# Kernel tuning notes

Hardware: AMD Instinct MI355X
Metric: run time of the kernel (lower is better)

Reference implementation:

```python
import jax, jax.numpy as jnp
import numpy as np

B, T, D = 2, 2048, 1024
H, G, K = 16, 4, 64          # num_heads, num_kv_heads, head_dim
R = H // G                   # GQA repeat factor
F = 4096                     # mlp_dim
EPS = 1e-6


def rms_norm(x, scale, eps=EPS):
    var = jnp.mean(x.astype(jnp.float32) ** 2, axis=-1, keepdims=True)
    normed = x * jax.lax.rsqrt(var + eps)
    return (scale * normed).astype(x.dtype)


def apply_rope(x_BTHK, sin_BTK, cos_BTK):
    half = x_BTHK.shape[-1] // 2
    x1, x2 = x_BTHK[..., :half], x_BTHK[..., half:]
    s = sin_BTK[:, :, None, :]
    c = cos_BTK[:, :, None, :]
    return jnp.concatenate([x1 * c - x2 * s, x2 * c + x1 * s], axis=-1).astype(x_BTHK.dtype)


def setup_inputs() -> dict:
    key = jax.random.key(0)
    ks = jax.random.split(key, 12)
    hidden_BTD = jax.random.normal(ks[0], (B, T, D), jnp.float32)
    # rope tables: realistic sin/cos of position*inv_freq
    inv_freq = 1.0 / (10000.0 ** (jnp.arange(K // 2, dtype=jnp.float32) / (K // 2)))
    ang = jnp.arange(T, dtype=jnp.float32)[:, None] * inv_freq[None, :]  # [T, K/2]
    sin_BTK = jnp.broadcast_to(jnp.sin(ang)[None], (B, T, K // 2))
    cos_BTK = jnp.broadcast_to(jnp.cos(ang)[None], (B, T, K // 2))
    mask = jnp.broadcast_to(jnp.tril(jnp.ones((T, T), bool))[None], (B, T, T))
    sc = 1.0 / np.sqrt(D)
    scf = 1.0 / np.sqrt(F)
    return {
        "hidden_BTD": hidden_BTD, "sin_BTK": sin_BTK, "cos_BTK": cos_BTK, "mask": mask,
        "ln1_scale": jnp.ones((D,), jnp.float32),
        "ln2_scale": jnp.ones((D,), jnp.float32),
        "qn_scale": jnp.ones((K,), jnp.float32),
        "kn_scale": jnp.ones((K,), jnp.float32),
        "q_w": jax.random.normal(ks[1], (D, H * K), jnp.float32) * sc,
        "k_w": jax.random.normal(ks[2], (D, G * K), jnp.float32) * sc,
        "v_w": jax.random.normal(ks[3], (D, G * K), jnp.float32) * sc,
        "o_w": jax.random.normal(ks[4], (H * K, D), jnp.float32) * sc,
        "gate_w": jax.random.normal(ks[5], (D, F), jnp.float32) * sc,
        "up_w": jax.random.normal(ks[6], (D, F), jnp.float32) * sc,
        "down_w": jax.random.normal(ks[7], (F, D), jnp.float32) * scf,
    }


def reference(hidden_BTD, sin_BTK, cos_BTK, mask, ln1_scale, ln2_scale,
              qn_scale, kn_scale, q_w, k_w, v_w, o_w, gate_w, up_w, down_w):
    x = rms_norm(hidden_BTD, ln1_scale)
    q = rms_norm((x @ q_w).reshape(B, T, H, K), qn_scale)
    k = rms_norm((x @ k_w).reshape(B, T, G, K), kn_scale)
    v = (x @ v_w).reshape(B, T, G, K)
    q = apply_rope(q, sin_BTK, cos_BTK)
    k = apply_rope(k, sin_BTK, cos_BTK)
    q_BTGRK = q.reshape(B, T, G, R, K)
    scale = K ** (-0.5)
    logits = jnp.einsum('BTGRK,BSGK->BTSGR', q_BTGRK, k) * scale
    neg = float(jnp.finfo(logits.dtype).min)
    logits = jnp.where(mask[:, :, :, None, None], logits, neg)
    weights = jax.nn.softmax(logits.astype(jnp.float32), axis=2).astype(logits.dtype)
    attn = jnp.einsum('BTSGR,BSGK->BTGRK', weights, v).reshape(B, T, H * K)
    hidden_BTD = hidden_BTD + attn @ o_w
    y = rms_norm(hidden_BTD, ln2_scale)
    ff = (jax.nn.silu(y @ gate_w) * (y @ up_w)) @ down_w
    return hidden_BTD + ff
```

## Files before the change

kernel.cpp:

```cpp
#include <hip/hip_runtime.h>
#include <hip/hip_bf16.h>

#define EPSF 1e-6f
constexpr int Bsz  = 2;
constexpr int Tseq = 2048;
constexpr int Dmod = 1024;
constexpr int Hh   = 16;
constexpr int Gg   = 4;
constexpr int Ff   = 4096;
constexpr int Mrows = Bsz * Tseq;

typedef __attribute__((ext_vector_type(8))) short bf16x8;
typedef __attribute__((ext_vector_type(4))) float f32x4;
typedef unsigned short u16;

__device__ inline u16 f2bf(float x) {
    union { float f; unsigned u; } v; v.f = x;
    unsigned r = v.u + 0x7fff + ((v.u >> 16) & 1);
    return (u16)(r >> 16);
}
__device__ inline float bf2f(u16 h) {
    union { unsigned u; float f; } v; v.u = ((unsigned)h) << 16; return v.f;
}

__device__ __forceinline__ void async_copy16(const u16* g, u16* l) {
    __builtin_amdgcn_global_load_lds(
        (const __attribute__((address_space(1))) void*)g,
        (__attribute__((address_space(3))) void*)l, 16, 0, 0);
}


__global__ __launch_bounds__(256) void wprep_all_kernel(
    const float* __restrict__ q_w, const float* __restrict__ k_w,
    const float* __restrict__ v_w, const float* __restrict__ o_w,
    const float* __restrict__ gate_w, const float* __restrict__ up_w,
    const float* __restrict__ down_w,
    u16* __restrict__ QKVT, u16* __restrict__ OTh, u16* __restrict__ OTl,
    u16* __restrict__ GTh, u16* __restrict__ UTh, u16* __restrict__ DTh)
{
    const int bx = blockIdx.x;
    const float* W; u16* Th; u16* Tl = nullptr;
    int N, Kd, ntile, ktile, drow;
    if (bx < 1024) {
        W = q_w; N = 1024; Kd = 1024; ntile = bx & 31; ktile = bx >> 5;
        Th = QKVT; drow = ntile * 32;
    } else if (bx < 1280) {
        const int i = bx - 1024;
        W = k_w; N = 256; Kd = 1024; ntile = i & 7; ktile = i >> 3;
        Th = QKVT; drow = 1024 + ntile * 32;
    } else if (bx < 1536) {
        const int i = bx - 1280;
        W = v_w; N = 256; Kd = 1024; ntile = i & 7; ktile = i >> 3;
        Th = QKVT; drow = 1280 + ntile * 32;
    } else if (bx < 2560) {
        const int i = bx - 1536;
        W = o_w; N = 1024; Kd = 1024; ntile = i & 31; ktile = i >> 5;
        Th = OTh; Tl = OTl; drow = ntile * 32;
    } else if (bx < 6656) {
        const int i = bx - 2560;
        W = gate_w; N = 4096; Kd = 1024; ntile = i & 127; ktile = i >> 7;
        Th = GTh; drow = ntile * 32;
    } else if (bx < 10752) {
        const int i = bx - 6656;
        W = up_w; N = 4096; Kd = 1024; ntile = i & 127; ktile = i >> 7;
        Th = UTh; drow = ntile * 32;
    } else {
        const int i = bx - 10752;
        W = down_w; N = 1024; Kd = 4096; ntile = i & 31; ktile = i >> 5;
        Th = DTh; drow = ntile * 32;
    }
    const int n0 = ntile * 32, k0 = ktile * 32;

    __shared__ float tile[32][33];
    const int r = threadIdx.x >> 3, c4 = (threadIdx.x & 7) * 4;
    const float4 v = *reinterpret_cast<const float4*>(&W[(size_t)(k0 + r) * N + n0 + c4]);
    tile[r][c4 + 0] = v.x; tile[r][c4 + 1] = v.y;
    tile[r][c4 + 2] = v.z; tile[r][c4 + 3] = v.w;
    __syncthreads();
    const int nl = threadIdx.x >> 3, kq = (threadIdx.x & 7) * 4;
    float x0 = tile[kq + 0][nl], x1 = tile[kq + 1][nl];
    float x2 = tile[kq + 2][nl], x3 = tile[kq + 3][nl];
    ushort4 h;
    h.x = f2bf(x0); h.y = f2bf(x1); h.z = f2bf(x2); h.w = f2bf(x3);
    *reinterpret_cast<ushort4*>(&Th[(size_t)(drow + nl) * Kd + k0 + kq]) = h;
    if (Tl) {
        ushort4 l;
        l.x = f2bf(x0 - bf2f(h.x)); l.y = f2bf(x1 - bf2f(h.y));
        l.z = f2bf(x2 - bf2f(h.z)); l.w = f2bf(x3 - bf2f(h.w));
        *reinterpret_cast<ushort4*>(&Tl[(size_t)(drow + nl) * Kd + k0 + kq]) = l;
    }
}

template <int LO>
__global__ __launch_bounds__(256) void rmsnorm_split_kernel(
    const float* __restrict__ x, const float* __restrict__ scale,
    u16* __restrict__ oh, u16* __restrict__ ol)
{
    const int row = blockIdx.x;
    const int tid = threadIdx.x;
    const float4 v = reinterpret_cast<const float4*>(x + (size_t)row * Dmod)[tid];
    float ss = v.x * v.x + v.y * v.y + v.z * v.z + v.w * v.w;
    #pragma unroll
    for (int off = 32; off; off >>= 1) ss += __shfl_xor(ss, off, 64);
    __shared__ float part[4];
    if ((tid & 63) == 0) part[tid >> 6] = ss;
    __syncthreads();
    const float tot = part[0] + part[1] + part[2] + part[3];
    const float rstd = rsqrtf(tot * (1.0f / Dmod) + EPSF);
    const float4 sc = reinterpret_cast<const float4*>(scale)[tid];
    float o0 = v.x * rstd * sc.x, o1 = v.y * rstd * sc.y;
    float o2 = v.z * rstd * sc.z, o3 = v.w * rstd * sc.w;
    ushort4 h;
    h.x = f2bf(o0); h.y = f2bf(o1); h.z = f2bf(o2); h.w = f2bf(o3);
    *reinterpret_cast<ushort4*>(&oh[(size_t)row * Dmod + tid * 4]) = h;
    if (LO) {
        ushort4 l;
        l.x = f2bf(o0 - bf2f(h.x)); l.y = f2bf(o1 - bf2f(h.y));
        l.z = f2bf(o2 - bf2f(h.z)); l.w = f2bf(o3 - bf2f(h.w));
        *reinterpret_cast<ushort4*>(&ol[(size_t)row * Dmod + tid * 4]) = l;
    }
}

template <int ASPLIT, int BSPLIT, int RES>
__global__ __launch_bounds__(256, 2) void mfma_gemm_kernel(
    const u16* __restrict__ Ah, const u16* __restrict__ Al,
    const u16* __restrict__ Bh, const u16* __restrict__ Bl,
    const float* __restrict__ res, float* __restrict__ C,
    int M, int N, int Kd)
{
    __shared__ u16 As_h[128 * 32];
    __shared__ u16 As_l[128 * 32];
    __shared__ u16 Bs_h[128 * 32];
    __shared__ u16 Bs_l[128 * 32];

    const int tid = threadIdx.x;
    const int lane = tid & 63, wave = tid >> 6;
    const int wm = (wave >> 1) * 64, wn = (wave & 1) * 64;
    const int m0 = blockIdx.y * 128, n0 = blockIdx.x * 128;
    const int fm = lane & 15, quad = lane >> 4;
    const int fsw = (fm >> 1) & 3;
    const int fcol = ((quad ^ fsw) * 8);

    f32x4 acc[4][4];
    #pragma unroll
    for (int i = 0; i < 4; ++i)
        #pragma unroll
        for (int j = 0; j < 4; ++j) acc[i][j] = (f32x4){0.f, 0.f, 0.f, 0.f};

    const int lrow = lane >> 2;
    const int lchunk = lane & 3;
    const int schunk = lchunk ^ ((lrow >> 1) & 3);

    for (int k0 = 0; k0 < Kd; k0 += 32) {
        __syncthreads();
        #pragma unroll
        for (int p = 0; p < 2; ++p) {
            const int row = wave * 32 + p * 16 + lrow;
            const size_t ga = (size_t)(m0 + row) * Kd + k0 + schunk * 8;
            const size_t gb = (size_t)(n0 + row) * Kd + k0 + schunk * 8;
            const int ls = row * 32 + lchunk * 8;
            async_copy16(&Ah[ga], &As_h[ls]);
            if (ASPLIT) async_copy16(&Al[ga], &As_l[ls]);
            async_copy16(&Bh[gb], &Bs_h[ls]);
            if (BSPLIT) async_copy16(&Bl[gb], &Bs_l[ls]);
        }
        __syncthreads();

        bf16x8 ah[4], al[4], bh[4], bl[4];
        #pragma unroll
        for (int t = 0; t < 4; ++t) {
            const int ra = (wm + t * 16 + fm) * 32 + fcol;
            const int rb = (wn + t * 16 + fm) * 32 + fcol;
            ah[t] = *reinterpret_cast<const bf16x8*>(&As_h[ra]);
            bh[t] = *reinterpret_cast<const bf16x8*>(&Bs_h[rb]);
            if (ASPLIT) al[t] = *reinterpret_cast<const bf16x8*>(&As_l[ra]);
            if (BSPLIT) bl[t] = *reinterpret_cast<const bf16x8*>(&Bs_l[rb]);
        }
        #pragma unroll
        for (int mt = 0; mt < 4; ++mt)
            #pragma unroll
            for (int nt = 0; nt < 4; ++nt) {
                acc[mt][nt] = __builtin_amdgcn_mfma_f32_16x16x32_bf16(
                    ah[mt], bh[nt], acc[mt][nt], 0, 0, 0);
                if (BSPLIT)
                    acc[mt][nt] = __builtin_amdgcn_mfma_f32_16x16x32_bf16(
                        ah[mt], bl[nt], acc[mt][nt], 0, 0, 0);
                if (ASPLIT)
                    acc[mt][nt] = __builtin_amdgcn_mfma_f32_16x16x32_bf16(
                        al[mt], bh[nt], acc[mt][nt], 0, 0, 0);
            }
    }

    const int cr = (lane >> 4) * 4, cn = lane & 15;
    #pragma unroll
    for (int mt = 0; mt < 4; ++mt)
        #pragma unroll
        for (int nt = 0; nt < 4; ++nt)
            #pragma unroll
            for (int r = 0; r < 4; ++r) {
                const int gm = m0 + wm + mt * 16 + cr + r;
                const int gn = n0 + wn + nt * 16 + cn;
                float v = acc[mt][nt][r];
                if (RES) v += res[(size_t)gm * N + gn];
                C[(size_t)gm * N + gn] = v;
            }
}

__global__ __launch_bounds__(256, 2) void qkv_fused_kernel(
    const u16* __restrict__ Ah, const u16* __restrict__ Bh,
    const float* __restrict__ qn, const float* __restrict__ kn,
    const float* __restrict__ sinp, const float* __restrict__ cosp,
    u16* __restrict__ Qbh, u16* __restrict__ Qbl,
    u16* __restrict__ Kbh, u16* __restrict__ Kbl,
    u16* __restrict__ Vth, u16* __restrict__ Vtl)
{
    __shared__ u16 As_h[128 * 32];
    __shared__ u16 Bs_h[128 * 32];

    const int Kd = 1024;
    const int tid = threadIdx.x;
    const int lane = tid & 63, wave = tid >> 6;
    const int wm = (wave >> 1) * 64, wn = (wave & 1) * 64;
    const int m0 = blockIdx.y * 128, n0 = blockIdx.x * 128;
    const int fm = lane & 15, quad = lane >> 4;
    const int fsw = (fm >> 1) & 3;
    const int fcol = ((quad ^ fsw) * 8);

    f32x4 acc[4][4];
    #pragma unroll
    for (int i = 0; i < 4; ++i)
        #pragma unroll
        for (int j = 0; j < 4; ++j) acc[i][j] = (f32x4){0.f, 0.f, 0.f, 0.f};

    const int lrow = lane >> 2;
    const int lchunk = lane & 3;
    const int schunk = lchunk ^ ((lrow >> 1) & 3);

    for (int k0 = 0; k0 < Kd; k0 += 32) {
        __syncthreads();
        #pragma unroll
        for (int p = 0; p < 2; ++p) {
            const int row = wave * 32 + p * 16 + lrow;
            const size_t ga = (size_t)(m0 + row) * Kd + k0 + schunk * 8;
            const size_t gb = (size_t)(n0 + row) * Kd + k0 + schunk * 8;
            const int ls = row * 32 + lchunk * 8;
            async_copy16(&Ah[ga], &As_h[ls]);
            async_copy16(&Bh[gb], &Bs_h[ls]);
        }
        __syncthreads();

        bf16x8 ah[4], bh[4];
        #pragma unroll
        for (int t = 0; t < 4; ++t) {
            ah[t] = *reinterpret_cast<const bf16x8*>(&As_h[(wm + t * 16 + fm) * 32 + fcol]);
            bh[t] = *reinterpret_cast<const bf16x8*>(&Bs_h[(wn + t * 16 + fm) * 32 + fcol]);
        }
        #pragma unroll
        for (int mt = 0; mt < 4; ++mt)
            #pragma unroll
            for (int nt = 0; nt < 4; ++nt)
                acc[mt][nt] = __builtin_amdgcn_mfma_f32_16x16x32_bf16(
                    ah[mt], bh[nt], acc[mt][nt], 0, 0, 0);
    }

    const int gn0 = n0 + wn;
    const int l15 = lane & 15;

    if (gn0 < 1280) {
        const bool isQ = (gn0 < 1024);
        const float* nsc = isQ ? qn : kn;
        const float osc = isQ ? 0.125f : 1.0f;
        u16* __restrict__ oh = isQ ? Qbh : Kbh;
        u16* __restrict__ ol = isQ ? Qbl : Kbl;
        const int rowstride = isQ ? 1024 : 256;
        const int colbase = isQ ? gn0 : gn0 - 1024;
        float sc[4];
        #pragma unroll
        for (int nt = 0; nt < 4; ++nt) sc[nt] = nsc[nt * 16 + l15];

        #pragma unroll
        for (int mt = 0; mt < 4; ++mt)
            #pragma unroll
            for (int r = 0; r < 4; ++r) {
                const int bt = m0 + wm + mt * 16 + quad * 4 + r;
                float v[4];
                #pragma unroll
                for (int nt = 0; nt < 4; ++nt) v[nt] = acc[mt][nt][r];
                float ss = v[0] * v[0] + v[1] * v[1] + v[2] * v[2] + v[3] * v[3];
                #pragma unroll
                for (int off = 1; off < 16; off <<= 1)
                    ss += __shfl_xor(ss, off, 16);
                const float rstd = rsqrtf(ss * (1.0f / 64.0f) + EPSF);
                float nv[4];
                #pragma unroll
                for (int nt = 0; nt < 4; ++nt) nv[nt] = v[nt] * rstd * sc[nt];
                const float s0 = sinp[bt * 32 + l15];
                const float c0 = cosp[bt * 32 + l15];
                const float s1 = sinp[bt * 32 + 16 + l15];
                const float c1 = cosp[bt * 32 + 16 + l15];
                float o[4];
                o[0] = (nv[0] * c0 - nv[2] * s0) * osc;
                o[1] = (nv[1] * c1 - nv[3] * s1) * osc;
                o[2] = (nv[2] * c0 + nv[0] * s0) * osc;
                o[3] = (nv[3] * c1 + nv[1] * s1) * osc;
                #pragma unroll
                for (int nt = 0; nt < 4; ++nt) {
                    const size_t off = (size_t)bt * rowstride + colbase + nt * 16 + l15;
                    const u16 hi = f2bf(o[nt]);
                    oh[off] = hi;
                    ol[off] = f2bf(o[nt] - bf2f(hi));
                }
            }
    } else {
        const int g = (gn0 - 1280) >> 6;
        const int b = (m0 + wm) >> 11;
        const int tb = ((m0 + wm) & 2047) + quad * 4;
        #pragma unroll
        for (int mt = 0; mt < 4; ++mt)
            #pragma unroll
            for (int nt = 0; nt < 4; ++nt) {
                const float v0 = acc[mt][nt][0], v1 = acc[mt][nt][1];
                const float v2 = acc[mt][nt][2], v3 = acc[mt][nt][3];
                ushort4 hv, lv;
                hv.x = f2bf(v0); hv.y = f2bf(v1); hv.z = f2bf(v2); hv.w = f2bf(v3);
                lv.x = f2bf(v0 - bf2f(hv.x)); lv.y = f2bf(v1 - bf2f(hv.y));
                lv.z = f2bf(v2 - bf2f(hv.z)); lv.w = f2bf(v3 - bf2f(hv.w));
                const size_t off =
                    ((size_t)((b * 4 + g) * 64 + nt * 16 + l15)) * Tseq + tb + mt * 16;
                *reinterpret_cast<ushort4*>(&Vth[off]) = hv;
                *reinterpret_cast<ushort4*>(&Vtl[off]) = lv;
            }
    }
}

__global__ __launch_bounds__(256, 2) void mfma_gateup_kernel(
    const u16* __restrict__ Ah, const u16* __restrict__ Al,
    const u16* __restrict__ Bg, const u16* __restrict__ Bu,
    u16* __restrict__ FF, int M, int N, int Kd)
{
    __shared__ u16 As_h[128 * 32];
    __shared__ u16 As_l[128 * 32];
    __shared__ u16 Gs[64 * 32];
    __shared__ u16 Us[64 * 32];

    const int tid = threadIdx.x;
    const int lane = tid & 63, wave = tid >> 6;
    const int wm = (wave >> 1) * 64, wn = (wave & 1) * 32;
    const int m0 = blockIdx.y * 128, n0 = blockIdx.x * 64;
    const int fm = lane & 15, quad = lane >> 4;
    const int fsw = (fm >> 1) & 3;
    const int fcol = ((quad ^ fsw) * 8);

    f32x4 accg[4][2], accu[4][2];
    #pragma unroll
    for (int i = 0; i < 4; ++i)
        #pragma unroll
        for (int j = 0; j < 2; ++j) {
            accg[i][j] = (f32x4){0.f, 0.f, 0.f, 0.f};
            accu[i][j] = (f32x4){0.f, 0.f, 0.f, 0.f};
        }

    const int lrow = lane >> 2;
    const int lchunk = lane & 3;
    const int schunk = lchunk ^ ((lrow >> 1) & 3);

    for (int k0 = 0; k0 < Kd; k0 += 32) {
        __syncthreads();
        #pragma unroll
        for (int p = 0; p < 2; ++p) {
            const int row = p * 64 + wave * 16 + lrow;
            const size_t ga = (size_t)(m0 + row) * Kd + k0 + schunk * 8;
            const int ls = row * 32 + lchunk * 8;
            async_copy16(&Ah[ga], &As_h[ls]);
            async_copy16(&Al[ga], &As_l[ls]);
        }
        {
            const int row = wave * 16 + lrow;
            const size_t gb = (size_t)(n0 + row) * Kd + k0 + schunk * 8;
            const int ls = row * 32 + lchunk * 8;
            async_copy16(&Bg[gb], &Gs[ls]);
            async_copy16(&Bu[gb], &Us[ls]);
        }
        __syncthreads();

        bf16x8 a_h[4], a_l[4], g_f[2], u_f[2];
        #pragma unroll
        for (int t = 0; t < 4; ++t) {
            const int ra = (wm + t * 16 + fm) * 32 + fcol;
            a_h[t] = *reinterpret_cast<const bf16x8*>(&As_h[ra]);
            a_l[t] = *reinterpret_cast<const bf16x8*>(&As_l[ra]);
        }
        #pragma unroll
        for (int j = 0; j < 2; ++j) {
            const int rb = (wn + j * 16 + fm) * 32 + fcol;
            g_f[j] = *reinterpret_cast<const bf16x8*>(&Gs[rb]);
            u_f[j] = *reinterpret_cast<const bf16x8*>(&Us[rb]);
        }
        #pragma unroll
        for (int mt = 0; mt < 4; ++mt)
            #pragma unroll
            for (int nt = 0; nt < 2; ++nt) {
                accg[mt][nt] = __builtin_amdgcn_mfma_f32_16x16x32_bf16(
                    a_h[mt], g_f[nt], accg[mt][nt], 0, 0, 0);
                accg[mt][nt] = __builtin_amdgcn_mfma_f32_16x16x32_bf16(
                    a_l[mt], g_f[nt], accg[mt][nt], 0, 0, 0);
                accu[mt][nt] = __builtin_amdgcn_mfma_f32_16x16x32_bf16(
                    a_h[mt], u_f[nt], accu[mt][nt], 0, 0, 0);
                accu[mt][nt] = __builtin_amdgcn_mfma_f32_16x16x32_bf16(
                    a_l[mt], u_f[nt], accu[mt][nt], 0, 0, 0);
            }
    }

    const int cr = (lane >> 4) * 4, cn = lane & 15;
    #pragma unroll
    for (int mt = 0; mt < 4; ++mt)
        #pragma unroll
        for (int nt = 0; nt < 2; ++nt)
            #pragma unroll
            for (int r = 0; r < 4; ++r) {
                const int gm = m0 + wm + mt * 16 + cr + r;
                const int gn = n0 + wn + nt * 16 + cn;
                const float g = accg[mt][nt][r];
                const float ff = (g / (1.0f + __expf(-g))) * accu[mt][nt][r];
                FF[(size_t)gm * N + gn] = f2bf(ff);
            }
}

__global__ __launch_bounds__(256) void attn_mfma_kernel(
    const u16* __restrict__ Qh, const u16* __restrict__ Ql,
    const u16* __restrict__ Kh, const u16* __restrict__ Kl,
    const u16* __restrict__ Vth, const u16* __restrict__ Vtl,
    u16* __restrict__ AOh, u16* __restrict__ AOl)
{
    __shared__ u16 KsH[64 * 72];
    __shared__ u16 KsL[64 * 72];
    __shared__ u16 VsH[64 * 72];
    __shared__ u16 VsL[64 * 72];
    __shared__ u16 Ps[4][16 * 72];

    const int tid = threadIdx.x;
    const int wave = tid >> 6, lane = tid & 63;
    const int l15 = lane & 15, quad = lane >> 4;

    const int bg = blockIdx.x & 7;
    const int b = bg >> 2, g = bg & 3;
    const int win = 127 - (blockIdx.x >> 3);
    const int t0 = win * 16;
    const int h = g * 4 + wave;

    bf16x8 qh[2], ql[2];
    {
        const size_t qrow = (size_t)(b * Tseq + t0 + l15) * 1024 + h * 64;
        #pragma unroll
        for (int ks = 0; ks < 2; ++ks) {
            qh[ks] = *reinterpret_cast<const bf16x8*>(&Qh[qrow + ks * 32 + quad * 8]);
            ql[ks] = *reinterpret_cast<const bf16x8*>(&Ql[qrow + ks * 32 + quad * 8]);
        }
    }

    const int srow = tid >> 2;
    const int scol = (tid & 3) * 16;
    const size_t kgb = (size_t)(b * Tseq) * 256 + g * 64 + scol;
    const size_t vgb = (size_t)(bg * 64 + srow) * Tseq + scol;

    const int nit = t0 / 64 + 1;

    uint4 ck0, ck1, cl0, cl1, cv0, cv1, cw0, cw1;
    {
        const size_t ka = kgb + (size_t)srow * 256;
        ck0 = *reinterpret_cast<const uint4*>(&Kh[ka]);
        ck1 = *reinterpret_cast<const uint4*>(&Kh[ka + 8]);
        cl0 = *reinterpret_cast<const uint4*>(&Kl[ka]);
        cl1 = *reinterpret_cast<const uint4*>(&Kl[ka + 8]);
        cv0 = *reinterpret_cast<const uint4*>(&Vth[vgb]);
        cv1 = *reinterpret_cast<const uint4*>(&Vth[vgb + 8]);
        cw0 = *reinterpret_cast<const uint4*>(&Vtl[vgb]);
        cw1 = *reinterpret_cast<const uint4*>(&Vtl[vgb + 8]);
    }

    f32x4 oacc[4];
    #pragma unroll
    for (int nt = 0; nt < 4; ++nt) oacc[nt] = (f32x4){0.f, 0.f, 0.f, 0.f};
    float m_r[4], l_r[4];
    #pragma unroll
    for (int r = 0; r < 4; ++r) { m_r[r] = -1e30f; l_r[r] = 0.0f; }

    u16* psw = &Ps[wave][0];
    const int lb = srow * 72 + scol;

    for (int it = 0; it < nit; ++it) {
        const int s0 = it * 64;
        const bool diag = (it == nit - 1);

        __syncthreads();
        *reinterpret_cast<uint4*>(&KsH[lb])     = ck0;
        *reinterpret_cast<uint4*>(&KsH[lb + 8]) = ck1;
        *reinterpret_cast<uint4*>(&KsL[lb])     = cl0;
        *reinterpret_cast<uint4*>(&KsL[lb + 8]) = cl1;
        *reinterpret_cast<uint4*>(&VsH[lb])     = cv0;
        *reinterpret_cast<uint4*>(&VsH[lb + 8]) = cv1;
        *reinterpret_cast<uint4*>(&VsL[lb])     = cw0;
        *reinterpret_cast<uint4*>(&VsL[lb + 8]) = cw1;
        if (it + 1 < nit) {
            const size_t ka = kgb + (size_t)(s0 + 64 + srow) * 256;
            ck0 = *reinterpret_cast<const uint4*>(&Kh[ka]);
            ck1 = *reinterpret_cast<const uint4*>(&Kh[ka + 8]);
            cl0 = *reinterpret_cast<const uint4*>(&Kl[ka]);
            cl1 = *reinterpret_cast<const uint4*>(&Kl[ka + 8]);
            const size_t va = vgb + s0 + 64;
            cv0 = *reinterpret_cast<const uint4*>(&Vth[va]);
            cv1 = *reinterpret_cast<const uint4*>(&Vth[va + 8]);
            cw0 = *reinterpret_cast<const uint4*>(&Vtl[va]);
            cw1 = *reinterpret_cast<const uint4*>(&Vtl[va + 8]);
        }
        __syncthreads();

        f32x4 sacc[4];
        #pragma unroll
        for (int nt = 0; nt < 4; ++nt) sacc[nt] = (f32x4){0.f, 0.f, 0.f, 0.f};

        #pragma unroll
        for (int ks = 0; ks < 2; ++ks) {
            bf16x8 kfh[4], kfl[4];
            #pragma unroll
            for (int nt = 0; nt < 4; ++nt) {
                const int a = (nt * 16 + l15) * 72 + ks * 32 + quad * 8;
                kfh[nt] = *reinterpret_cast<const bf16x8*>(&KsH[a]);
                kfl[nt] = *reinterpret_cast<const bf16x8*>(&KsL[a]);
            }
            #pragma unroll
            for (int nt = 0; nt < 4; ++nt) {
                sacc[nt] = __builtin_amdgcn_mfma_f32_16x16x32_bf16(qh[ks], kfh[nt], sacc[nt], 0, 0, 0);
                sacc[nt] = __builtin_amdgcn_mfma_f32_16x16x32_bf16(ql[ks], kfh[nt], sacc[nt], 0, 0, 0);
                sacc[nt] = __builtin_amdgcn_mfma_f32_16x16x32_bf16(qh[ks], kfl[nt], sacc[nt], 0, 0, 0);
            }
        }

        if (diag) {
            #pragma unroll
            for (int nt = 0; nt < 4; ++nt) {
                const int sg = s0 + nt * 16 + l15;
                #pragma unroll
                for (int r = 0; r < 4; ++r)
                    if (sg > t0 + quad * 4 + r) sacc[nt][r] = -1e30f;
            }
        }

        #pragma unroll
        for (int r = 0; r < 4; ++r) {
            float mx = fmaxf(fmaxf(sacc[0][r], sacc[1][r]),
                             fmaxf(sacc[2][r], sacc[3][r]));
            #pragma unroll
            for (int off = 1; off < 16; off <<= 1)
                mx = fmaxf(mx, __shfl_xor(mx, off, 16));
            const float mnew = fmaxf(m_r[r], mx);
            const float alpha = __expf(m_r[r] - mnew);
            m_r[r] = mnew;

            float rs = 0.0f;
            #pragma unroll
            for (int nt = 0; nt < 4; ++nt) {
                const float p = __expf(sacc[nt][r] - mnew);
                sacc[nt][r] = p;
                rs += p;
            }
            #pragma unroll
            for (int off = 1; off < 16; off <<= 1)
                rs += __shfl_xor(rs, off, 16);
            l_r[r] = l_r[r] * alpha + rs;
            #pragma unroll
            for (int nt = 0; nt < 4; ++nt) oacc[nt][r] *= alpha;
            #pragma unroll
            for (int nt = 0; nt < 4; ++nt)
                psw[(quad * 4 + r) * 72 + nt * 16 + l15] = f2bf(sacc[nt][r]);
        }

        #pragma unroll
        for (int ks = 0; ks < 2; ++ks) {
            const bf16x8 pa = *reinterpret_cast<const bf16x8*>(
                &psw[l15 * 72 + ks * 32 + quad * 8]);
            bf16x8 vfh[4], vfl[4];
            #pragma unroll
            for (int nt = 0; nt < 4; ++nt) {
                const int a = (nt * 16 + l15) * 72 + ks * 32 + quad * 8;
                vfh[nt] = *reinterpret_cast<const bf16x8*>(&VsH[a]);
                vfl[nt] = *reinterpret_cast<const bf16x8*>(&VsL[a]);
            }
            #pragma unroll
            for (int nt = 0; nt < 4; ++nt) {
                oacc[nt] = __builtin_amdgcn_mfma_f32_16x16x32_bf16(pa, vfh[nt], oacc[nt], 0, 0, 0);
                oacc[nt] = __builtin_amdgcn_mfma_f32_16x16x32_bf16(pa, vfl[nt], oacc[nt], 0, 0, 0);
            }
        }
    }

    #pragma unroll
    for (int r = 0; r < 4; ++r) {
        const float inv = 1.0f / l_r[r];
        const size_t orow = (size_t)(b * Tseq + t0 + quad * 4 + r) * 1024 + h * 64;
        #pragma unroll
        for (int nt = 0; nt < 4; ++nt) {
            const float o = oacc[nt][r] * inv;
            const u16 hi = f2bf(o);
            AOh[orow + nt * 16 + l15] = hi;
            AOl[orow + nt * 16 + l15] = f2bf(o - bf2f(hi));
        }
    }
}

extern "C" void kernel_launch(void* const* d_in, const int* in_sizes, int n_in,
                              void* d_out, int out_size, void* d_ws,
                              size_t ws_size, hipStream_t stream)
{
    const float* hidden = (const float*)d_in[0];
    const float* sinp   = (const float*)d_in[1];
    const float* cosp   = (const float*)d_in[2];
    const float* ln1    = (const float*)d_in[4];
    const float* ln2    = (const float*)d_in[5];
    const float* qn     = (const float*)d_in[6];
    const float* kn     = (const float*)d_in[7];
    const float* q_w    = (const float*)d_in[8];
    const float* k_w    = (const float*)d_in[9];
    const float* v_w    = (const float*)d_in[10];
    const float* o_w    = (const float*)d_in[11];
    const float* gate_w = (const float*)d_in[12];
    const float* up_w   = (const float*)d_in[13];
    const float* down_w = (const float*)d_in[14];
    float* out = (float*)d_out;

    char* base = (char*)d_ws;
    u16*   OTh  = (u16*)(base);
    u16*   OTl  = (u16*)(base + 2097152);
    u16*   GTh  = (u16*)(base + 4194304);
    u16*   UTh  = (u16*)(base + 12582912);
    u16*   DTh  = (u16*)(base + 20971520);
    u16*   QKVT = (u16*)(base + 29360128);
    u16*   Xh   = (u16*)(base + 32505856);
    u16*   Qbh  = (u16*)(base + 40894464);
    u16*   Qbl  = (u16*)(base + 49283072);
    u16*   Kbh  = (u16*)(base + 57671680);
    u16*   Kbl  = (u16*)(base + 59768832);
    u16*   Vth  = (u16*)(base + 61865984);
    u16*   Vtl  = (u16*)(base + 63963136);
    u16*   AOh  = (u16*)(base + 66060288);
    u16*   AOl  = (u16*)(base + 74448896);
    u16*   FFh  = (u16*)(base + 82837504);

    float* H2 = (float*)Qbh;
    u16*   Yh = Kbh;
    u16*   Yl = AOh;

    wprep_all_kernel<<<14848, 256, 0, stream>>>(
        q_w, k_w, v_w, o_w, gate_w, up_w, down_w,
        QKVT, OTh, OTl, GTh, UTh, DTh);

    rmsnorm_split_kernel<0><<<Mrows, 256, 0, stream>>>(hidden, ln1, Xh, nullptr);

    qkv_fused_kernel<<<dim3(12, 32), 256, 0, stream>>>(
        Xh, QKVT, qn, kn, sinp, cosp, Qbh, Qbl, Kbh, Kbl, Vth, Vtl);

    attn_mfma_kernel<<<Bsz * Gg * (Tseq / 16), 256, 0, stream>>>(
        Qbh, Qbl, Kbh, Kbl, Vth, Vtl, AOh, AOl);

    mfma_gemm_kernel<1, 1, 1><<<dim3(8, 32), 256, 0, stream>>>(
        AOh, AOl, OTh, OTl, hidden, H2, Mrows, Dmod, 1024);

    rmsnorm_split_kernel<1><<<Mrows, 256, 0, stream>>>(H2, ln2, Yh, Yl);

    mfma_gateup_kernel<<<dim3(Ff / 64, Mrows / 128), 256, 0, stream>>>(
        Yh, Yl, GTh, UTh, FFh, Mrows, Ff, 1024);

    mfma_gemm_kernel<0, 0, 1><<<dim3(8, 32), 256, 0, stream>>>(
        FFh, nullptr, DTh, nullptr, H2, out, Mrows, Dmod, 4096);
}
```

Before: 532.4 us.

## Narrow GEMM tiles to 128x64 and XOR-swizzle attention LDS with higher occupancy

The o-proj and down-proj GEMMs now use 128x64 output tiles, giving twice as many blocks (512 rather than 256) for better CU fill on the 1024-wide outputs. Their shared arrays for the unused low halves shrink when that split is off. The attention kernel drops its padded 72-stride LDS layout for a 64-stride XOR-swizzled layout for K, V and P, and raises launch bounds to 4 blocks per CU. The aim is lower LDS use and higher occupancy without bank conflicts. The trade-off is less data reuse per GEMM tile and possible register pressure from the tighter launch bound.

Result: slower. 625.2 us (+17.4%).

```diff
diff --git a/kernel.cpp b/kernel.cpp
--- a/kernel.cpp
+++ b/kernel.cpp
@@ -122,30 +122,30 @@
 }
 
 template <int ASPLIT, int BSPLIT, int RES>
-__global__ __launch_bounds__(256, 2) void mfma_gemm_kernel(
+__global__ __launch_bounds__(256, 2) void mfma_gemm64_kernel(
     const u16* __restrict__ Ah, const u16* __restrict__ Al,
     const u16* __restrict__ Bh, const u16* __restrict__ Bl,
     const float* __restrict__ res, float* __restrict__ C,
     int M, int N, int Kd)
 {
     __shared__ u16 As_h[128 * 32];
-    __shared__ u16 As_l[128 * 32];
-    __shared__ u16 Bs_h[128 * 32];
-    __shared__ u16 Bs_l[128 * 32];
+    __shared__ u16 As_l[ASPLIT ? 128 * 32 : 8];
+    __shared__ u16 Bs_h[64 * 32];
+    __shared__ u16 Bs_l[BSPLIT ? 64 * 32 : 8];
 
     const int tid = threadIdx.x;
     const int lane = tid & 63, wave = tid >> 6;
-    const int wm = (wave >> 1) * 64, wn = (wave & 1) * 64;
-    const int m0 = blockIdx.y * 128, n0 = blockIdx.x * 128;
+    const int wm = (wave >> 1) * 64, wn = (wave & 1) * 32;
+    const int m0 = blockIdx.y * 128, n0 = blockIdx.x * 64;
     const int fm = lane & 15, quad = lane >> 4;
     const int fsw = (fm >> 1) & 3;
     const int fcol = ((quad ^ fsw) * 8);
 
-    f32x4 acc[4][4];
+    f32x4 acc[4][2];
     #pragma unroll
     for (int i = 0; i < 4; ++i)
         #pragma unroll
-        for (int j = 0; j < 4; ++j) acc[i][j] = (f32x4){0.f, 0.f, 0.f, 0.f};
+        for (int j = 0; j < 2; ++j) acc[i][j] = (f32x4){0.f, 0.f, 0.f, 0.f};
 
     const int lrow = lane >> 2;
     const int lchunk = lane & 3;
@@ -155,39 +155,46 @@
         __syncthreads();
         #pragma unroll
         for (int p = 0; p < 2; ++p) {
-            const int row = wave * 32 + p * 16 + lrow;
+            const int row = p * 64 + wave * 16 + lrow;
             const size_t ga = (size_t)(m0 + row) * Kd + k0 + schunk * 8;
-            const size_t gb = (size_t)(n0 + row) * Kd + k0 + schunk * 8;
             const int ls = row * 32 + lchunk * 8;
             async_copy16(&Ah[ga], &As_h[ls]);
             if (ASPLIT) async_copy16(&Al[ga], &As_l[ls]);
+        }
+        {
+            const int row = wave * 16 + lrow;
+            const size_t gb = (size_t)(n0 + row) * Kd + k0 + schunk * 8;
+            const int ls = row * 32 + lchunk * 8;
             async_copy16(&Bh[gb], &Bs_h[ls]);
             if (BSPLIT) async_copy16(&Bl[gb], &Bs_l[ls]);
         }
         __syncthreads();
 
-        bf16x8 ah[4], al[4], bh[4], bl[4];
+        bf16x8 a_h[4], a_l[4], b_h[2], b_l[2];
         #pragma unroll
         for (int t = 0; t < 4; ++t) {
             const int ra = (wm + t * 16 + fm) * 32 + fcol;
-            const int rb = (wn + t * 16 + fm) * 32 + fcol;
-            ah[t] = *reinterpret_cast<const bf16x8*>(&As_h[ra]);
-            bh[t] = *reinterpret_cast<const bf16x8*>(&Bs_h[rb]);
-            if (ASPLIT) al[t] = *reinterpret_cast<const bf16x8*>(&As_l[ra]);
-            if (BSPLIT) bl[t] = *reinterpret_cast<const bf16x8*>(&Bs_l[rb]);
+            a_h[t] = *reinterpret_cast<const bf16x8*>(&As_h[ra]);
+            if (ASPLIT) a_l[t] = *reinterpret_cast<const bf16x8*>(&As_l[ra]);
+        }
+        #pragma unroll
+        for (int j = 0; j < 2; ++j) {
+            const int rb = (wn + j * 16 + fm) * 32 + fcol;
+            b_h[j] = *reinterpret_cast<const bf16x8*>(&Bs_h[rb]);
+            if (BSPLIT) b_l[j] = *reinterpret_cast<const bf16x8*>(&Bs_l[rb]);
         }
         #pragma unroll
         for (int mt = 0; mt < 4; ++mt)
             #pragma unroll
-            for (int nt = 0; nt < 4; ++nt) {
+            for (int nt = 0; nt < 2; ++nt) {
                 acc[mt][nt] = __builtin_amdgcn_mfma_f32_16x16x32_bf16(
-                    ah[mt], bh[nt], acc[mt][nt], 0, 0, 0);
+                    a_h[mt], b_h[nt], acc[mt][nt], 0, 0, 0);
                 if (BSPLIT)
                     acc[mt][nt] = __builtin_amdgcn_mfma_f32_16x16x32_bf16(
-                        ah[mt], bl[nt], acc[mt][nt], 0, 0, 0);
+                        a_h[mt], b_l[nt], acc[mt][nt], 0, 0, 0);
                 if (ASPLIT)
                     acc[mt][nt] = __builtin_amdgcn_mfma_f32_16x16x32_bf16(
-                        al[mt], bh[nt], acc[mt][nt], 0, 0, 0);
+                        a_l[mt], b_h[nt], acc[mt][nt], 0, 0, 0);
             }
     }
 
@@ -195,7 +202,7 @@
     #pragma unroll
     for (int mt = 0; mt < 4; ++mt)
         #pragma unroll
-        for (int nt = 0; nt < 4; ++nt)
+        for (int nt = 0; nt < 2; ++nt)
             #pragma unroll
             for (int r = 0; r < 4; ++r) {
                 const int gm = m0 + wm + mt * 16 + cr + r;
@@ -426,21 +433,22 @@
             }
 }
 
-__global__ __launch_bounds__(256) void attn_mfma_kernel(
+__global__ __launch_bounds__(256, 4) void attn_mfma_kernel(
     const u16* __restrict__ Qh, const u16* __restrict__ Ql,
     const u16* __restrict__ Kh, const u16* __restrict__ Kl,
     const u16* __restrict__ Vth, const u16* __restrict__ Vtl,
     u16* __restrict__ AOh, u16* __restrict__ AOl)
 {
-    __shared__ u16 KsH[64 * 72];
-    __shared__ u16 KsL[64 * 72];
-    __shared__ u16 VsH[64 * 72];
-    __shared__ u16 VsL[64 * 72];
-    __shared__ u16 Ps[4][16 * 72];
+    __shared__ u16 KsH[64 * 64];
+    __shared__ u16 KsL[64 * 64];
+    __shared__ u16 VsH[64 * 64];
+    __shared__ u16 VsL[64 * 64];
+    __shared__ u16 Ps[4][16 * 64];
 
     const int tid = threadIdx.x;
     const int wave = tid >> 6, lane = tid & 63;
     const int l15 = lane & 15, quad = lane >> 4;
+    const int fsw7 = l15 & 7;
 
     const int bg = blockIdx.x & 7;
     const int b = bg >> 2, g = bg & 3;
@@ -459,9 +467,12 @@
     }
 
     const int srow = tid >> 2;
-    const int scol = (tid & 3) * 16;
-    const size_t kgb = (size_t)(b * Tseq) * 256 + g * 64 + scol;
-    const size_t vgb = (size_t)(bg * 64 + srow) * Tseq + scol;
+    const int j2 = (tid & 3) * 2;
+    const int sw = srow & 7;
+    const int d0 = srow * 64 + ((j2    ) ^ sw) * 8;
+    const int d1 = srow * 64 + ((j2 + 1) ^ sw) * 8;
+    const size_t kgb = (size_t)(b * Tseq) * 256 + g * 64 + j2 * 8;
+    const size_t vgb = (size_t)(bg * 64 + srow) * Tseq + j2 * 8;
 
     const int nit = t0 / 64 + 1;
 
@@ -486,21 +497,20 @@
     for (int r = 0; r < 4; ++r) { m_r[r] = -1e30f; l_r[r] = 0.0f; }
 
     u16* psw = &Ps[wave][0];
-    const int lb = srow * 72 + scol;
 
     for (int it = 0; it < nit; ++it) {
         const int s0 = it * 64;
         const bool diag = (it == nit - 1);
 
         __syncthreads();
-        *reinterpret_cast<uint4*>(&KsH[lb])     = ck0;
-        *reinterpret_cast<uint4*>(&KsH[lb + 8]) = ck1;
-        *reinterpret_cast<uint4*>(&KsL[lb])     = cl0;
-        *reinterpret_cast<uint4*>(&KsL[lb + 8]) = cl1;
-        *reinterpret_cast<uint4*>(&VsH[lb])     = cv0;
-        *reinterpret_cast<uint4*>(&VsH[lb + 8]) = cv1;
-        *reinterpret_cast<uint4*>(&VsL[lb])     = cw0;
-        *reinterpret_cast<uint4*>(&VsL[lb + 8]) = cw1;
+        *reinterpret_cast<uint4*>(&KsH[d0]) = ck0;
+        *reinterpret_cast<uint4*>(&KsH[d1]) = ck1;
+        *reinterpret_cast<uint4*>(&KsL[d0]) = cl0;
+        *reinterpret_cast<uint4*>(&KsL[d1]) = cl1;
+        *reinterpret_cast<uint4*>(&VsH[d0]) = cv0;
+        *reinterpret_cast<uint4*>(&VsH[d1]) = cv1;
+        *reinterpret_cast<uint4*>(&VsL[d0]) = cw0;
+        *reinterpret_cast<uint4*>(&VsL[d1]) = cw1;
         if (it + 1 < nit) {
             const size_t ka = kgb + (size_t)(s0 + 64 + srow) * 256;
             ck0 = *reinterpret_cast<const uint4*>(&Kh[ka]);
@@ -521,10 +531,11 @@
 
         #pragma unroll
         for (int ks = 0; ks < 2; ++ks) {
+            const int pc = ((ks * 4 + quad) ^ fsw7) * 8;
             bf16x8 kfh[4], kfl[4];
             #pragma unroll
             for (int nt = 0; nt < 4; ++nt) {
-                const int a = (nt * 16 + l15) * 72 + ks * 32 + quad * 8;
+                const int a = (nt * 16 + l15) * 64 + pc;
                 kfh[nt] = *reinterpret_cast<const bf16x8*>(&KsH[a]);
                 kfl[nt] = *reinterpret_cast<const bf16x8*>(&KsL[a]);
             }
@@ -570,19 +581,25 @@
             l_r[r] = l_r[r] * alpha + rs;
             #pragma unroll
             for (int nt = 0; nt < 4; ++nt) oacc[nt][r] *= alpha;
-            #pragma unroll
-            for (int nt = 0; nt < 4; ++nt)
-                psw[(quad * 4 + r) * 72 + nt * 16 + l15] = f2bf(sacc[nt][r]);
+            const int prow = quad * 4 + r;
+            const int prs = prow & 7;
+            #pragma unroll
+            for (int nt = 0; nt < 4; ++nt) {
+                const int lc = nt * 2 + (l15 >> 3);
+                psw[prow * 64 + ((lc ^ prs) << 3) + (l15 & 7)] =
+                    f2bf(sacc[nt][r]);
+            }
         }
 
         #pragma unroll
         for (int ks = 0; ks < 2; ++ks) {
             const bf16x8 pa = *reinterpret_cast<const bf16x8*>(
-                &psw[l15 * 72 + ks * 32 + quad * 8]);
+                &psw[l15 * 64 + (((ks * 4 + quad) ^ fsw7) << 3)]);
+            const int pc = ((ks * 4 + quad) ^ fsw7) * 8;
             bf16x8 vfh[4], vfl[4];
             #pragma unroll
             for (int nt = 0; nt < 4; ++nt) {
-                const int a = (nt * 16 + l15) * 72 + ks * 32 + quad * 8;
+                const int a = (nt * 16 + l15) * 64 + pc;
                 vfh[nt] = *reinterpret_cast<const bf16x8*>(&VsH[a]);
                 vfl[nt] = *reinterpret_cast<const bf16x8*>(&VsL[a]);
             }
@@ -662,7 +679,7 @@
     attn_mfma_kernel<<<Bsz * Gg * (Tseq / 16), 256, 0, stream>>>(
         Qbh, Qbl, Kbh, Kbl, Vth, Vtl, AOh, AOl);
 
-    mfma_gemm_kernel<1, 1, 1><<<dim3(8, 32), 256, 0, stream>>>(
+    mfma_gemm64_kernel<1, 1, 1><<<dim3(16, 32), 256, 0, stream>>>(
         AOh, AOl, OTh, OTl, hidden, H2, Mrows, Dmod, 1024);
 
     rmsnorm_split_kernel<1><<<Mrows, 256, 0, stream>>>(H2, ln2, Yh, Yl);
@@ -670,6 +687,6 @@
     mfma_gateup_kernel<<<dim3(Ff / 64, Mrows / 128), 256, 0, stream>>>(
         Yh, Yl, GTh, UTh, FFh, Mrows, Ff, 1024);
 
-    mfma_gemm_kernel<0, 0, 1><<<dim3(8, 32), 256, 0, stream>>>(
+    mfma_gemm64_kernel<0, 0, 1><<<dim3(16, 32), 256, 0, stream>>>(
         FFh, nullptr, DTh, nullptr, H2, out, Mrows, Dmod, 4096);
 }
```
